# Performance work log

Hardware: AMD Instinct MI355X
Metric: run time of the kernel (lower is better)

The kernel has to match this reference:

```python
import jax, jax.numpy as jnp
import numpy as np

B, S, H = 2, 2048, 1024          # batch, seq, hidden_size
I = 512                          # expert_ffn_hidden_size
E_R, E_Z = 32, 8                 # routed experts, zero (identity) experts
E_T = E_R + E_Z                  # total experts
K = 6                            # moe_topk
SCALE = 2.5                      # routed_scaling_factor
W_INIT = 0.02


def setup_inputs() -> dict:
    key = jax.random.key(0)
    k0, k1, k2, k3 = jax.random.split(key, 4)
    return {
        "hidden_states": jax.random.normal(k0, (B, S, H), jnp.float32),
        "classifier_weight": jax.random.normal(k1, (E_T, H), jnp.float32) * W_INIT,
        "e_score_correction_bias": jnp.zeros((E_T,), jnp.float32),
        "gate_up_proj": jax.random.normal(k2, (E_T, 2 * I, H), jnp.float32) * W_INIT,
        "down_proj": jax.random.normal(k3, (E_R, H, I), jnp.float32) * W_INIT,
    }


def reference(hidden_states, classifier_weight, e_score_correction_bias,
              gate_up_proj, down_proj):
    orig_shape = hidden_states.shape
    x = hidden_states.reshape(-1, H).astype(jnp.float32)      # [T, H]
    T = x.shape[0]

    # ---- router (fp32 like the torch code) ----
    logits = x @ classifier_weight.T                          # [T, E_T]
    scores = jax.nn.softmax(logits, axis=-1)
    _, topk_idx = jax.lax.top_k(scores + e_score_correction_bias[None, :], K)
    topk_w = jnp.take_along_axis(scores, topk_idx, axis=1) * SCALE  # [T, K]

    # dense per-(token, expert) combine weights; 0 for unselected experts
    w_full = jnp.zeros((T, E_T), jnp.float32).at[
        jnp.arange(T)[:, None], topk_idx].add(topk_w)          # [T, E_T]

    # zero experts: weighted identity
    zero_w = w_full[:, E_R:].sum(axis=-1, keepdims=True)       # [T, 1]
    out0 = x * zero_w

    # routed experts: SwiGLU MLP per expert, scanned over experts
    routed_w = w_full[:, :E_R].T                               # [E_R, T]

    def body(out, xs):
        Wgu, Wd, we = xs                                       # [2I,H],[H,I],[T]
        gate, up = jnp.split(x @ Wgu.T, 2, axis=-1)            # [T, I] each
        y = (jax.nn.silu(gate) * up) @ Wd.T                    # [T, H]
        return out + we[:, None] * y, None

    out, _ = jax.lax.scan(body, out0, (gate_up_proj[:E_R], down_proj, routed_w))
    return out.reshape(orig_shape).astype(hidden_states.dtype)
```

## Files before the change

kernel.cpp:

```cpp
#include <hip/hip_runtime.h>
#include <float.h>
#include <math.h>

#define TT 4096
#define HH 1024
#define II 512
#define E_R 32
#define E_T 40
#define TOPK 6
#define SCALE_F 2.5f
#define MAXTILES 224

typedef __bf16 bf16x8 __attribute__((ext_vector_type(8)));
typedef float f32x4 __attribute__((ext_vector_type(4)));

__device__ inline unsigned short f2bf(float f) {
  __bf16 h = (__bf16)f;
  return __builtin_bit_cast(unsigned short, h);
}

__device__ inline uint4 cvt8(float4 a, float4 b) {
  bf16x8 v;
  v[0] = (__bf16)a.x; v[1] = (__bf16)a.y; v[2] = (__bf16)a.z; v[3] = (__bf16)a.w;
  v[4] = (__bf16)b.x; v[5] = (__bf16)b.y; v[6] = (__bf16)b.z; v[7] = (__bf16)b.w;
  return __builtin_bit_cast(uint4, v);
}

__device__ inline void gload_lds16(const void* g, void* l) {
  __builtin_amdgcn_global_load_lds(
      (__attribute__((address_space(1))) void*)g,
      (__attribute__((address_space(3))) void*)l, 16, 0, 0);
}

__device__ inline void lds_store16(unsigned short* base, int row, int c8, uint4 v) {
  int byte = (row * 128 + c8 * 16) ^ ((row & 7) << 4);
  *reinterpret_cast<uint4*>(reinterpret_cast<char*>(base) + byte) = v;
}
__device__ inline bf16x8 lds_frag(const unsigned short* base, int row, int kb) {
  int byte = (row * 128 + kb * 2) ^ ((row & 7) << 4);
  uint4 v = *reinterpret_cast<const uint4*>(reinterpret_cast<const char*>(base) + byte);
  return __builtin_bit_cast(bf16x8, v);
}

__device__ inline f32x4 mfma16(bf16x8 a, bf16x8 b, f32x4 c) {
  return __builtin_amdgcn_mfma_f32_16x16x32_bf16(a, b, c, 0, 0, 0);
}

__global__ void k_convert_x(const float* __restrict__ x, unsigned short* __restrict__ xb) {
  int i = blockIdx.x * 256 + threadIdx.x;
  const float4* p = reinterpret_cast<const float4*>(x) + (size_t)i * 2;
  float4 a = p[0], b = p[1];
  reinterpret_cast<uint4*>(xb)[i] = cvt8(a, b);
}

__global__ __launch_bounds__(256) void k_logits(const float* __restrict__ x,
                                                const float* __restrict__ wcls,
                                                float* __restrict__ logits) {
  __shared__ float4 ws4[E_T * 64];
  const int tid = threadIdx.x;
  const int lane = tid & 63;
  const int wave = tid >> 6;
  const int token = blockIdx.x * 4 + wave;
  const float4* x4 = reinterpret_cast<const float4*>(x);
  const float4* w4 = reinterpret_cast<const float4*>(wcls);

  float acc[E_T];
  #pragma unroll
  for (int e = 0; e < E_T; ++e) acc[e] = 0.f;

  for (int c = 0; c < 4; ++c) {
    if (c) __syncthreads();
    #pragma unroll
    for (int j = 0; j < 10; ++j) {
      int v = tid + j * 256;
      int e = v >> 6, kq = v & 63;
      ws4[v] = w4[e * 256 + c * 64 + kq];
    }
    float4 xv = x4[(size_t)token * 256 + c * 64 + lane];
    __syncthreads();
    #pragma unroll
    for (int e = 0; e < E_T; ++e) {
      float4 w = ws4[e * 64 + lane];
      acc[e] += xv.x * w.x + xv.y * w.y + xv.z * w.z + xv.w * w.w;
    }
  }

  float mine = 0.f;
  #pragma unroll
  for (int e = 0; e < E_T; ++e) {
    float r = acc[e];
    #pragma unroll
    for (int o = 32; o; o >>= 1) r += __shfl_xor(r, o);
    if (lane == e) mine = r;
  }
  if (lane < E_T) logits[(size_t)token * E_T + lane] = mine;
}

__global__ void k_topk(const float* __restrict__ logits, const float* __restrict__ bias,
                       float* __restrict__ zero_w, int* __restrict__ counts,
                       int* __restrict__ tok_list, float* __restrict__ wt_list) {
  int t = blockIdx.x * 64 + threadIdx.x;
  float l[E_T];
  const float4* lp = reinterpret_cast<const float4*>(logits + (size_t)t * E_T);
  #pragma unroll
  for (int j = 0; j < E_T / 4; ++j) {
    float4 v = lp[j];
    l[j * 4 + 0] = v.x; l[j * 4 + 1] = v.y; l[j * 4 + 2] = v.z; l[j * 4 + 3] = v.w;
  }
  float m = -FLT_MAX;
  #pragma unroll
  for (int e = 0; e < E_T; ++e) m = fmaxf(m, l[e]);
  float den = 0.f;
  #pragma unroll
  for (int e = 0; e < E_T; ++e) { l[e] = __expf(l[e] - m); den += l[e]; }
  float inv = 1.f / den;
  float sel[E_T];
  #pragma unroll
  for (int e = 0; e < E_T; ++e) { l[e] *= inv; sel[e] = l[e] + bias[e]; }

  unsigned long long used = 0ull;
  float zw = 0.f;
  for (int k = 0; k < TOPK; ++k) {
    float bv = -FLT_MAX; int bj = 0;
    #pragma unroll
    for (int e = 0; e < E_T; ++e) {
      float v = ((used >> e) & 1ull) ? -FLT_MAX : sel[e];
      if (v > bv) { bv = v; bj = e; }
    }
    used |= 1ull << bj;
    float wgt = (bv - bias[bj]) * SCALE_F;
    if (bj >= E_R) {
      zw += wgt;
    } else {
      int p = atomicAdd(&counts[bj], 1);
      tok_list[bj * TT + p] = t;
      wt_list[bj * TT + p] = wgt;
    }
  }
  zero_w[t] = zw;
}

__global__ void k_scan(const int* __restrict__ counts, int* __restrict__ offsets,
                       int* __restrict__ tiles) {
  if (threadIdx.x == 0) {
    int s = 0, idx = 0;
    for (int e = 0; e < E_R; ++e) {
      offsets[e] = s;
      int c = counts[e];
      s += c;
      for (int r0 = 0; r0 < c; r0 += 128) tiles[1 + idx++] = (e << 16) | r0;
    }
    offsets[E_R] = s;
    tiles[0] = idx;
  }
}

__global__ void k_init_out(const float* __restrict__ x, const float* __restrict__ zero_w,
                           float* __restrict__ out) {
  int i = blockIdx.x * 256 + threadIdx.x;
  int t = i >> 8;
  float zw = zero_w[t];
  float4 v = reinterpret_cast<const float4*>(x)[i];
  v.x *= zw; v.y *= zw; v.z *= zw; v.w *= zw;
  reinterpret_cast<float4*>(out)[i] = v;
}

__global__ __launch_bounds__(512, 4) void k_gemm1(
    const unsigned short* __restrict__ xb, const float* __restrict__ gup,
    const int* __restrict__ tok_list, const int* __restrict__ counts,
    const int* __restrict__ offsets, const int* __restrict__ tiles,
    unsigned short* __restrict__ inter) {
  const int nt = tiles[0];
  if ((int)blockIdx.y >= nt) return;
  const int tv = tiles[1 + blockIdx.y];
  const int e = tv >> 16;
  const int row0 = tv & 0xffff;
  const int cnt = counts[e];
  const int off = offsets[e];
  const int n0 = blockIdx.x * 64;
  const int tid = threadIdx.x;
  const int lane = tid & 63;
  const int wave = tid >> 6;
  const int wr = wave >> 2;
  const int wcol = wave & 3;

  __shared__ __align__(16) unsigned short lA[128 * 64];
  __shared__ __align__(16) unsigned short lBg[64 * 64];
  __shared__ __align__(16) unsigned short lBu[64 * 64];
  __shared__ int toks[128];

  if (tid < 128) {
    int r = row0 + tid;
    toks[tid] = tok_list[e * TT + (r < cnt ? r : cnt - 1)];
  }
  __syncthreads();

  size_t asrc[2];
  #pragma unroll
  for (int i = 0; i < 2; ++i) {
    int lrow = wave * 16 + i * 8 + (lane >> 3);
    asrc[i] = (size_t)toks[lrow] * HH + (((lane & 7) ^ (lrow & 7)) * 8);
  }
  const int brow = tid >> 3, bc8 = tid & 7;
  const float4* bgp = reinterpret_cast<const float4*>(
      gup + ((size_t)e * 1024 + n0 + brow) * HH) + bc8 * 2;
  const float4* bup = reinterpret_cast<const float4*>(
      gup + ((size_t)e * 1024 + 512 + n0 + brow) * HH) + bc8 * 2;

  f32x4 accg[4] = {}; f32x4 accu[4] = {};

  for (int k0 = 0; k0 < HH; k0 += 64) {
    int kq = k0 >> 2;
    #pragma unroll
    for (int i = 0; i < 2; ++i)
      gload_lds16(xb + asrc[i] + k0, lA + (wave * 16 + i * 8) * 64);
    {
      float4 ga = bgp[kq], gb = bgp[kq + 1];
      lds_store16(lBg, brow, bc8, cvt8(ga, gb));
      float4 ua = bup[kq], ub = bup[kq + 1];
      lds_store16(lBu, brow, bc8, cvt8(ua, ub));
    }
    __syncthreads();
    #pragma unroll
    for (int ks = 0; ks < 2; ++ks) {
      int kb = ks * 32 + ((lane >> 4) << 3);
      bf16x8 g = lds_frag(lBg, wcol * 16 + (lane & 15), kb);
      bf16x8 u = lds_frag(lBu, wcol * 16 + (lane & 15), kb);
      #pragma unroll
      for (int i = 0; i < 4; ++i) {
        bf16x8 a = lds_frag(lA, wr * 64 + i * 16 + (lane & 15), kb);
        accg[i] = mfma16(a, g, accg[i]);
        accu[i] = mfma16(a, u, accu[i]);
      }
    }
    __syncthreads();
  }

  #pragma unroll
  for (int i = 0; i < 4; ++i)
    #pragma unroll
    for (int r = 0; r < 4; ++r) {
      int rloc = wr * 64 + i * 16 + ((lane >> 4) << 2) + r;
      int grow = row0 + rloc;
      if (grow < cnt) {
        int col = n0 + wcol * 16 + (lane & 15);
        float gv = accg[i][r], uv = accu[i][r];
        float act = gv / (1.f + __expf(-gv)) * uv;
        inter[(size_t)(off + grow) * II + col] = f2bf(act);
      }
    }
}

__global__ __launch_bounds__(512, 4) void k_gemm2(
    const unsigned short* __restrict__ inter, const float* __restrict__ dwn,
    const int* __restrict__ tok_list, const float* __restrict__ wt_list,
    const int* __restrict__ counts, const int* __restrict__ offsets,
    const int* __restrict__ tiles, float* __restrict__ out) {
  const int nt = tiles[0];
  if ((int)blockIdx.y >= nt) return;
  const int tv = tiles[1 + blockIdx.y];
  const int e = tv >> 16;
  const int row0 = tv & 0xffff;
  const int cnt = counts[e];
  const int off = offsets[e];
  const int h0 = blockIdx.x * 128;
  const int tid = threadIdx.x;
  const int lane = tid & 63;
  const int wave = tid >> 6;
  const int wr = wave >> 2;
  const int wc = wave & 3;

  __shared__ __align__(16) unsigned short lA[128 * 64];
  __shared__ __align__(16) unsigned short lB[128 * 64];
  __shared__ int toks[128];
  __shared__ float wts[128];

  if (tid < 128) {
    int r = row0 + tid;
    int rc = r < cnt ? r : cnt - 1;
    toks[tid] = tok_list[e * TT + rc];
    wts[tid] = (r < cnt) ? wt_list[e * TT + rc] : 0.f;
  }
  __syncthreads();

  size_t asrc[2];
  #pragma unroll
  for (int i = 0; i < 2; ++i) {
    int lrow = wave * 16 + i * 8 + (lane >> 3);
    int rr = row0 + lrow; rr = rr < cnt ? rr : cnt - 1;
    asrc[i] = (size_t)(off + rr) * II + (((lane & 7) ^ (lrow & 7)) * 8);
  }
  int brow[2], bc8[2];
  const float4* bp[2];
  #pragma unroll
  for (int s = 0; s < 2; ++s) {
    int idx = tid + s * 512;
    brow[s] = idx >> 3; bc8[s] = idx & 7;
    bp[s] = reinterpret_cast<const float4*>(
        dwn + ((size_t)e * HH + h0 + brow[s]) * II) + bc8[s] * 2;
  }

  f32x4 acc[4][2] = {};

  for (int k0 = 0; k0 < II; k0 += 64) {
    int kq = k0 >> 2;
    #pragma unroll
    for (int i = 0; i < 2; ++i)
      gload_lds16(inter + asrc[i] + k0, lA + (wave * 16 + i * 8) * 64);
    #pragma unroll
    for (int s = 0; s < 2; ++s) {
      float4 a = bp[s][kq], b = bp[s][kq + 1];
      lds_store16(lB, brow[s], bc8[s], cvt8(a, b));
    }
    __syncthreads();
    #pragma unroll
    for (int ks = 0; ks < 2; ++ks) {
      int kb = ks * 32 + ((lane >> 4) << 3);
      bf16x8 b0 = lds_frag(lB, wc * 32 + (lane & 15), kb);
      bf16x8 b1 = lds_frag(lB, wc * 32 + 16 + (lane & 15), kb);
      #pragma unroll
      for (int i = 0; i < 4; ++i) {
        bf16x8 a = lds_frag(lA, wr * 64 + i * 16 + (lane & 15), kb);
        acc[i][0] = mfma16(a, b0, acc[i][0]);
        acc[i][1] = mfma16(a, b1, acc[i][1]);
      }
    }
    __syncthreads();
  }

  #pragma unroll
  for (int i = 0; i < 4; ++i)
    #pragma unroll
    for (int j = 0; j < 2; ++j)
      #pragma unroll
      for (int r = 0; r < 4; ++r) {
        int rloc = wr * 64 + i * 16 + ((lane >> 4) << 2) + r;
        int grow = row0 + rloc;
        if (grow < cnt) {
          int h = h0 + wc * 32 + j * 16 + (lane & 15);
          unsafeAtomicAdd(&out[(size_t)toks[rloc] * HH + h], acc[i][j][r] * wts[rloc]);
        }
      }
}


extern "C" void kernel_launch(void* const* d_in, const int* in_sizes, int n_in,
                              void* d_out, int out_size, void* d_ws, size_t ws_size,
                              hipStream_t stream) {
  const float* x    = (const float*)d_in[0];
  const float* wcls = (const float*)d_in[1];
  const float* bias = (const float*)d_in[2];
  const float* gup  = (const float*)d_in[3];
  const float* dwn  = (const float*)d_in[4];
  float* out = (float*)d_out;

  char* w = (char*)d_ws;
  unsigned short* xb    = (unsigned short*)(w + 0);
  float* zero_w         = (float*)(w + 8388608);
  int* counts           = (int*)(w + 8404992);
  int* offsets          = (int*)(w + 8405120);
  int* tok_list         = (int*)(w + 8405376);
  float* wt_list        = (float*)(w + 8929664);
  float* logits         = (float*)(w + 9453952);
  int* tiles            = (int*)(w + 10109312);
  unsigned short* inter = (unsigned short*)(w + 10113408);

  hipMemsetAsync(counts, 0, E_R * sizeof(int), stream);
  k_convert_x<<<2048, 256, 0, stream>>>(x, xb);
  k_logits<<<1024, 256, 0, stream>>>(x, wcls, logits);
  k_topk<<<64, 64, 0, stream>>>(logits, bias, zero_w, counts, tok_list, wt_list);
  k_scan<<<1, 64, 0, stream>>>(counts, offsets, tiles);
  k_init_out<<<4096, 256, 0, stream>>>(x, zero_w, out);
  k_gemm1<<<dim3(8, MAXTILES), 512, 0, stream>>>(xb, gup, tok_list, counts, offsets, tiles, inter);
  k_gemm2<<<dim3(8, MAXTILES), 512, 0, stream>>>(inter, dwn, tok_list, wt_list, counts, offsets, tiles, out);
}
```

Baseline: 256.7 us.

## Double-buffer LDS in expert GEMMs and replace atomic scatter with gather combine

```diff
diff --git a/kernel.cpp b/kernel.cpp
--- a/kernel.cpp
+++ b/kernel.cpp
@@ -98,7 +98,9 @@
 
 __global__ void k_topk(const float* __restrict__ logits, const float* __restrict__ bias,
                        float* __restrict__ zero_w, int* __restrict__ counts,
-                       int* __restrict__ tok_list, float* __restrict__ wt_list) {
+                       int* __restrict__ tok_list,
+                       int* __restrict__ route_ep, float* __restrict__ route_w,
+                       int* __restrict__ route_n) {
   int t = blockIdx.x * 64 + threadIdx.x;
   float l[E_T];
   const float4* lp = reinterpret_cast<const float4*>(logits + (size_t)t * E_T);
@@ -120,6 +122,7 @@
 
   unsigned long long used = 0ull;
   float zw = 0.f;
+  int nr = 0;
   for (int k = 0; k < TOPK; ++k) {
     float bv = -FLT_MAX; int bj = 0;
     #pragma unroll
@@ -134,10 +137,13 @@
     } else {
       int p = atomicAdd(&counts[bj], 1);
       tok_list[bj * TT + p] = t;
-      wt_list[bj * TT + p] = wgt;
+      route_ep[t * TOPK + nr] = (bj << 16) | p;
+      route_w[t * TOPK + nr] = wgt;
+      nr++;
     }
   }
   zero_w[t] = zw;
+  route_n[t] = nr;
 }
 
 __global__ void k_scan(const int* __restrict__ counts, int* __restrict__ offsets,
@@ -153,16 +159,6 @@
     offsets[E_R] = s;
     tiles[0] = idx;
   }
-}
-
-__global__ void k_init_out(const float* __restrict__ x, const float* __restrict__ zero_w,
-                           float* __restrict__ out) {
-  int i = blockIdx.x * 256 + threadIdx.x;
-  int t = i >> 8;
-  float zw = zero_w[t];
-  float4 v = reinterpret_cast<const float4*>(x)[i];
-  v.x *= zw; v.y *= zw; v.z *= zw; v.w *= zw;
-  reinterpret_cast<float4*>(out)[i] = v;
 }
 
 __global__ __launch_bounds__(512, 4) void k_gemm1(
@@ -184,9 +180,9 @@
   const int wr = wave >> 2;
   const int wcol = wave & 3;
 
-  __shared__ __align__(16) unsigned short lA[128 * 64];
-  __shared__ __align__(16) unsigned short lBg[64 * 64];
-  __shared__ __align__(16) unsigned short lBu[64 * 64];
+  __shared__ __align__(16) unsigned short lA0[128 * 64], lA1[128 * 64];
+  __shared__ __align__(16) unsigned short lBg0[64 * 64], lBg1[64 * 64];
+  __shared__ __align__(16) unsigned short lBu0[64 * 64], lBu1[64 * 64];
   __shared__ int toks[128];
 
   if (tid < 128) {
@@ -209,29 +205,50 @@
 
   f32x4 accg[4] = {}; f32x4 accu[4] = {};
 
-  for (int k0 = 0; k0 < HH; k0 += 64) {
-    int kq = k0 >> 2;
+  {
     #pragma unroll
     for (int i = 0; i < 2; ++i)
-      gload_lds16(xb + asrc[i] + k0, lA + (wave * 16 + i * 8) * 64);
-    {
-      float4 ga = bgp[kq], gb = bgp[kq + 1];
-      lds_store16(lBg, brow, bc8, cvt8(ga, gb));
-      float4 ua = bup[kq], ub = bup[kq + 1];
-      lds_store16(lBu, brow, bc8, cvt8(ua, ub));
-    }
-    __syncthreads();
+      gload_lds16(xb + asrc[i], lA0 + (wave * 16 + i * 8) * 64);
+    float4 ga = bgp[0], gb = bgp[1], ua = bup[0], ub = bup[1];
+    lds_store16(lBg0, brow, bc8, cvt8(ga, gb));
+    lds_store16(lBu0, brow, bc8, cvt8(ua, ub));
+  }
+  __syncthreads();
+
+  for (int t = 0; t < 16; ++t) {
+    const bool last = (t == 15);
+    unsigned short* cA  = (t & 1) ? lA1 : lA0;
+    unsigned short* cBg = (t & 1) ? lBg1 : lBg0;
+    unsigned short* cBu = (t & 1) ? lBu1 : lBu0;
+    unsigned short* nA  = (t & 1) ? lA0 : lA1;
+    unsigned short* nBg = (t & 1) ? lBg0 : lBg1;
+    unsigned short* nBu = (t & 1) ? lBu0 : lBu1;
+
+    float4 ga, gb, ua, ub;
+    if (!last) {
+      int k1 = (t + 1) * 64, kq = k1 >> 2;
+      #pragma unroll
+      for (int i = 0; i < 2; ++i)
+        gload_lds16(xb + asrc[i] + k1, nA + (wave * 16 + i * 8) * 64);
+      ga = bgp[kq]; gb = bgp[kq + 1]; ua = bup[kq]; ub = bup[kq + 1];
+    }
+
     #pragma unroll
     for (int ks = 0; ks < 2; ++ks) {
       int kb = ks * 32 + ((lane >> 4) << 3);
-      bf16x8 g = lds_frag(lBg, wcol * 16 + (lane & 15), kb);
-      bf16x8 u = lds_frag(lBu, wcol * 16 + (lane & 15), kb);
+      bf16x8 g = lds_frag(cBg, wcol * 16 + (lane & 15), kb);
+      bf16x8 u = lds_frag(cBu, wcol * 16 + (lane & 15), kb);
       #pragma unroll
       for (int i = 0; i < 4; ++i) {
-        bf16x8 a = lds_frag(lA, wr * 64 + i * 16 + (lane & 15), kb);
+        bf16x8 a = lds_frag(cA, wr * 64 + i * 16 + (lane & 15), kb);
         accg[i] = mfma16(a, g, accg[i]);
         accu[i] = mfma16(a, u, accu[i]);
       }
+    }
+
+    if (!last) {
+      lds_store16(nBg, brow, bc8, cvt8(ga, gb));
+      lds_store16(nBu, brow, bc8, cvt8(ua, ub));
     }
     __syncthreads();
   }
@@ -253,9 +270,8 @@
 
 __global__ __launch_bounds__(512, 4) void k_gemm2(
     const unsigned short* __restrict__ inter, const float* __restrict__ dwn,
-    const int* __restrict__ tok_list, const float* __restrict__ wt_list,
     const int* __restrict__ counts, const int* __restrict__ offsets,
-    const int* __restrict__ tiles, float* __restrict__ out) {
+    const int* __restrict__ tiles, unsigned short* __restrict__ inter2) {
   const int nt = tiles[0];
   if ((int)blockIdx.y >= nt) return;
   const int tv = tiles[1 + blockIdx.y];
@@ -270,18 +286,8 @@
   const int wr = wave >> 2;
   const int wc = wave & 3;
 
-  __shared__ __align__(16) unsigned short lA[128 * 64];
-  __shared__ __align__(16) unsigned short lB[128 * 64];
-  __shared__ int toks[128];
-  __shared__ float wts[128];
-
-  if (tid < 128) {
-    int r = row0 + tid;
-    int rc = r < cnt ? r : cnt - 1;
-    toks[tid] = tok_list[e * TT + rc];
-    wts[tid] = (r < cnt) ? wt_list[e * TT + rc] : 0.f;
-  }
-  __syncthreads();
+  __shared__ __align__(16) unsigned short lA0[128 * 64], lA1[128 * 64];
+  __shared__ __align__(16) unsigned short lB0[128 * 64], lB1[128 * 64];
 
   size_t asrc[2];
   #pragma unroll
@@ -302,28 +308,52 @@
 
   f32x4 acc[4][2] = {};
 
-  for (int k0 = 0; k0 < II; k0 += 64) {
-    int kq = k0 >> 2;
+  {
     #pragma unroll
     for (int i = 0; i < 2; ++i)
-      gload_lds16(inter + asrc[i] + k0, lA + (wave * 16 + i * 8) * 64);
+      gload_lds16(inter + asrc[i], lA0 + (wave * 16 + i * 8) * 64);
     #pragma unroll
     for (int s = 0; s < 2; ++s) {
-      float4 a = bp[s][kq], b = bp[s][kq + 1];
-      lds_store16(lB, brow[s], bc8[s], cvt8(a, b));
-    }
-    __syncthreads();
+      float4 a = bp[s][0], b = bp[s][1];
+      lds_store16(lB0, brow[s], bc8[s], cvt8(a, b));
+    }
+  }
+  __syncthreads();
+
+  for (int t = 0; t < 8; ++t) {
+    const bool last = (t == 7);
+    unsigned short* cA = (t & 1) ? lA1 : lA0;
+    unsigned short* cB = (t & 1) ? lB1 : lB0;
+    unsigned short* nA = (t & 1) ? lA0 : lA1;
+    unsigned short* nB = (t & 1) ? lB0 : lB1;
+
+    float4 pa[2], pb[2];
+    if (!last) {
+      int k1 = (t + 1) * 64, kq = k1 >> 2;
+      #pragma unroll
+      for (int i = 0; i < 2; ++i)
+        gload_lds16(inter + asrc[i] + k1, nA + (wave * 16 + i * 8) * 64);
+      #pragma unroll
+      for (int s = 0; s < 2; ++s) { pa[s] = bp[s][kq]; pb[s] = bp[s][kq + 1]; }
+    }
+
     #pragma unroll
     for (int ks = 0; ks < 2; ++ks) {
       int kb = ks * 32 + ((lane >> 4) << 3);
-      bf16x8 b0 = lds_frag(lB, wc * 32 + (lane & 15), kb);
-      bf16x8 b1 = lds_frag(lB, wc * 32 + 16 + (lane & 15), kb);
+      bf16x8 b0 = lds_frag(cB, wc * 32 + (lane & 15), kb);
+      bf16x8 b1 = lds_frag(cB, wc * 32 + 16 + (lane & 15), kb);
       #pragma unroll
       for (int i = 0; i < 4; ++i) {
-        bf16x8 a = lds_frag(lA, wr * 64 + i * 16 + (lane & 15), kb);
+        bf16x8 a = lds_frag(cA, wr * 64 + i * 16 + (lane & 15), kb);
         acc[i][0] = mfma16(a, b0, acc[i][0]);
         acc[i][1] = mfma16(a, b1, acc[i][1]);
       }
+    }
+
+    if (!last) {
+      #pragma unroll
+      for (int s = 0; s < 2; ++s)
+        lds_store16(nB, brow[s], bc8[s], cvt8(pa[s], pb[s]));
     }
     __syncthreads();
   }
@@ -338,9 +368,33 @@
         int grow = row0 + rloc;
         if (grow < cnt) {
           int h = h0 + wc * 32 + j * 16 + (lane & 15);
-          unsafeAtomicAdd(&out[(size_t)toks[rloc] * HH + h], acc[i][j][r] * wts[rloc]);
+          inter2[(size_t)(off + grow) * HH + h] = f2bf(acc[i][j][r]);
         }
       }
+}
+
+__global__ __launch_bounds__(256) void k_combine(
+    const float* __restrict__ x, const float* __restrict__ zero_w,
+    const int* __restrict__ offsets, const int* __restrict__ route_ep,
+    const float* __restrict__ route_w, const int* __restrict__ route_n,
+    const unsigned short* __restrict__ inter2, float* __restrict__ out) {
+  const int t = blockIdx.x;
+  const int tid = threadIdx.x;
+  const float zw = zero_w[t];
+  const int n = route_n[t];
+  float4 o = reinterpret_cast<const float4*>(x)[t * 256 + tid];
+  o.x *= zw; o.y *= zw; o.z *= zw; o.w *= zw;
+  for (int i = 0; i < n; ++i) {
+    int ep = route_ep[t * TOPK + i];
+    int row = offsets[ep >> 16] + (ep & 0xffff);
+    float w = route_w[t * TOPK + i];
+    ushort4 v = reinterpret_cast<const ushort4*>(inter2 + (size_t)row * HH)[tid];
+    o.x += w * __builtin_bit_cast(float, (unsigned)v.x << 16);
+    o.y += w * __builtin_bit_cast(float, (unsigned)v.y << 16);
+    o.z += w * __builtin_bit_cast(float, (unsigned)v.z << 16);
+    o.w += w * __builtin_bit_cast(float, (unsigned)v.w << 16);
+  }
+  reinterpret_cast<float4*>(out)[t * 256 + tid] = o;
 }
 
 
@@ -360,17 +414,22 @@
   int* counts           = (int*)(w + 8404992);
   int* offsets          = (int*)(w + 8405120);
   int* tok_list         = (int*)(w + 8405376);
-  float* wt_list        = (float*)(w + 8929664);
-  float* logits         = (float*)(w + 9453952);
-  int* tiles            = (int*)(w + 10109312);
-  unsigned short* inter = (unsigned short*)(w + 10113408);
+  float* logits         = (float*)(w + 8929664);
+  int* tiles            = (int*)(w + 9585024);
+  int* route_ep         = (int*)(w + 9589120);
+  float* route_w        = (float*)(w + 9687424);
+  int* route_n          = (int*)(w + 9785728);
+  unsigned short* inter = (unsigned short*)(w + 9802112);
+  unsigned short* inter2 = (unsigned short*)(w + 34967936);
 
   hipMemsetAsync(counts, 0, E_R * sizeof(int), stream);
   k_convert_x<<<2048, 256, 0, stream>>>(x, xb);
   k_logits<<<1024, 256, 0, stream>>>(x, wcls, logits);
-  k_topk<<<64, 64, 0, stream>>>(logits, bias, zero_w, counts, tok_list, wt_list);
+  k_topk<<<64, 64, 0, stream>>>(logits, bias, zero_w, counts, tok_list,
+                                route_ep, route_w, route_n);
   k_scan<<<1, 64, 0, stream>>>(counts, offsets, tiles);
-  k_init_out<<<4096, 256, 0, stream>>>(x, zero_w, out);
   k_gemm1<<<dim3(8, MAXTILES), 512, 0, stream>>>(xb, gup, tok_list, counts, offsets, tiles, inter);
-  k_gemm2<<<dim3(8, MAXTILES), 512, 0, stream>>>(inter, dwn, tok_list, wt_list, counts, offsets, tiles, out);
-}
+  k_gemm2<<<dim3(8, MAXTILES), 512, 0, stream>>>(inter, dwn, counts, offsets, tiles, inter2);
+  k_combine<<<TT, 256, 0, stream>>>(x, zero_w, offsets, route_ep, route_w, route_n,
+                                    inter2, out);
+}
```

Result: no change. 254.2 us (-1.0%).
